# Kernel tuning notes

Hardware: AMD Instinct MI355X
Metric: run time of the kernel (lower is better)

## Reference

```python
import jax, jax.numpy as jnp
import numpy as np

HEADS, DIM_HEAD, C, B, HS, WS = 8, 64, 512, 2, 48, 48


def setup_inputs() -> dict:
    key = jax.random.key(0)
    ks = jax.random.split(key, 9)
    s = 0.02
    return {
        "hidden_states": jax.random.normal(ks[0], (B, C, HS, WS), jnp.float32),
        "Wq": jax.random.normal(ks[1], (HEADS, DIM_HEAD, C), jnp.float32) * s,
        "bq": jax.random.normal(ks[2], (HEADS, DIM_HEAD), jnp.float32) * s,
        "Wk": jax.random.normal(ks[3], (HEADS, DIM_HEAD, C), jnp.float32) * s,
        "bk": jax.random.normal(ks[4], (HEADS, DIM_HEAD), jnp.float32) * s,
        "Wv": jax.random.normal(ks[5], (HEADS, DIM_HEAD, C), jnp.float32) * s,
        "bv": jax.random.normal(ks[6], (HEADS, DIM_HEAD), jnp.float32) * s,
        "Wo": jax.random.normal(ks[7], (C, HEADS * DIM_HEAD), jnp.float32) * s,
        "bo": jax.random.normal(ks[8], (C,), jnp.float32) * s,
    }


def reference(hidden_states, Wq, bq, Wk, bk, Wv, bv, Wo, bo):
    # hidden_states: [B, C, H, W]; per-head 1x1 convs == per-head linear over C.
    b, c, h, w = hidden_states.shape
    hw = h * w
    x = hidden_states.reshape(b, c, hw)  # [B, C, HW]
    # Batched per-head projections (fuses the per-head Conv2d loop).
    q = jnp.einsum('bcs,ndc->bnsd', x, Wq) + bq[None, :, None, :]  # [B, n, HW, d]
    k = jnp.einsum('bcs,ndc->bnsd', x, Wk) + bk[None, :, None, :]
    v = jnp.einsum('bcs,ndc->bnsd', x, Wv) + bv[None, :, None, :]
    scale = 1.0 / jnp.sqrt(jnp.asarray(DIM_HEAD, hidden_states.dtype))
    scores = jnp.einsum('bnqd,bnkd->bnqk', q, k) * scale  # [B, n, HW, HW]
    probs = jax.nn.softmax(scores, axis=-1)
    attn = jnp.einsum('bnqk,bnkd->bnqd', probs, v)  # [B, n, HW, d]
    # concat heads along last dim (matches torch.cat(..., dim=-1))
    attn = attn.transpose(0, 2, 1, 3).reshape(b, hw, HEADS * DIM_HEAD)
    out = attn @ Wo.T + bo  # [B, HW, C] (to_out[0]; to_out[1] dropout = identity)
    out = out.reshape(b, h, w, c).transpose(0, 3, 1, 2)  # [B, C, H, W]
    return out
```

## Files before the change

kernel.cpp:

```cpp
#include <hip/hip_runtime.h>
#include <hip/hip_bf16.h>

#define HEADS 8
#define DHEAD 64
#define CDIM  512
#define SEQ   2304
#define ND    512
#define NCHUNK 4

typedef unsigned short u16;
typedef unsigned int   u32;
typedef __attribute__((ext_vector_type(8))) short short8;
typedef __attribute__((ext_vector_type(4))) float f32x4;

#define QSCALE 0.18033688011112043f

__device__ __forceinline__ u16 f2bf(float f) {
    union { float f; u32 u; } x; x.f = f;
    u32 r = x.u + 0x7FFFu + ((x.u >> 16) & 1u);
    return (u16)(r >> 16);
}
__device__ __forceinline__ float bf2f(u16 v) {
    union { u32 u; float f; } x; x.u = ((u32)v) << 16; return x.f;
}
__device__ __forceinline__ u32 pkbf(float a, float b) {
    union { float f; u32 u; } x, y; x.f = a; y.f = b;
    return __builtin_amdgcn_perm(y.u + 0x8000u, x.u + 0x8000u, 0x07060302u);
}
__device__ __forceinline__ u32 cvtpk(float lo, float hi) {
    u32 r;
    asm("v_cvt_pk_bf16_f32 %0, %1, %2" : "=v"(r) : "v"(lo), "v"(hi));
    return r;
}
__device__ __forceinline__ f32x4 mfma16(short8 a, short8 b, f32x4 c) {
    return __builtin_amdgcn_mfma_f32_16x16x32_bf16(a, b, c, 0, 0, 0);
}
__device__ __forceinline__ void cp16(const void* g, void* l) {
    __builtin_amdgcn_global_load_lds(
        (const __attribute__((address_space(1))) u32*)(uintptr_t)g,
        (__attribute__((address_space(3))) u32*)(u32)(uintptr_t)l,
        16, 0, 0);
}
__device__ __forceinline__ int kperm_inv(int r) {
    return (r & ~0x1C) | ((r & 0x0C) << 1) | ((r & 0x10) >> 2);
}

__global__ void prep_kernel(const float* __restrict__ H,
                            const float* __restrict__ Wq, const float* __restrict__ Wk,
                            const float* __restrict__ Wv, const float* __restrict__ Wo,
                            u16* __restrict__ Wqkv, u16* __restrict__ Wob,
                            u16* __restrict__ X) {
    __shared__ float tile[64][65];
    const int t = threadIdx.x;
    const int bx = blockIdx.x;
    if (bx < 512) {
        const int N1 = CDIM * ND;
        int i8 = (bx * 256 + t) * 8;
        const float* src;
        u16* dst;
        if (i8 < 3 * N1) {
            src = (i8 < N1) ? &Wq[i8] : (i8 < 2 * N1 ? &Wk[i8 - N1] : &Wv[i8 - 2 * N1]);
            dst = &Wqkv[i8];
        } else {
            src = &Wo[i8 - 3 * N1];
            dst = &Wob[i8 - 3 * N1];
        }
        float4 a = *(const float4*)src;
        float4 c = *(const float4*)(src + 4);
        uint4 o;
        o.x = pkbf(a.x, a.y); o.y = pkbf(a.z, a.w);
        o.z = pkbf(c.x, c.y); o.w = pkbf(c.z, c.w);
        *(uint4*)dst = o;
    } else {
        int bb = bx - 512;
        int st = bb % 36, ct = (bb / 36) % 8, b = bb / (36 * 8);
#pragma unroll
        for (int it = 0; it < 4; ++it) {
            int cl = it * 16 + (t >> 4);
            int j4 = (t & 15) * 4;
            float4 hv = *(const float4*)&H[((size_t)(b * CDIM + ct * 64 + cl)) * SEQ + st * 64 + j4];
            tile[cl][j4 + 0] = hv.x; tile[cl][j4 + 1] = hv.y;
            tile[cl][j4 + 2] = hv.z; tile[cl][j4 + 3] = hv.w;
        }
        __syncthreads();
        int sl = t >> 2, c16 = (t & 3) * 16;
        uint4 o1, o2;
        o1.x = cvtpk(tile[c16 +  0][sl], tile[c16 +  1][sl]);
        o1.y = cvtpk(tile[c16 +  2][sl], tile[c16 +  3][sl]);
        o1.z = cvtpk(tile[c16 +  4][sl], tile[c16 +  5][sl]);
        o1.w = cvtpk(tile[c16 +  6][sl], tile[c16 +  7][sl]);
        o2.x = cvtpk(tile[c16 +  8][sl], tile[c16 +  9][sl]);
        o2.y = cvtpk(tile[c16 + 10][sl], tile[c16 + 11][sl]);
        o2.z = cvtpk(tile[c16 + 12][sl], tile[c16 + 13][sl]);
        o2.w = cvtpk(tile[c16 + 14][sl], tile[c16 + 15][sl]);
        u16* xp = &X[((size_t)(b * SEQ + st * 64 + sl)) * CDIM + ct * 64 + c16];
        *(uint4*)xp = o1;
        *(uint4*)(xp + 8) = o2;
    }
}

__global__ __launch_bounds__(256, 2) void gemm_qkv_kernel(
        const u16* __restrict__ W, const u16* __restrict__ X,
        const float* __restrict__ bq, const float* __restrict__ bk, const float* __restrict__ bv,
        u16* __restrict__ Q, u16* __restrict__ K, u16* __restrict__ V) {
    __shared__ __align__(16) u16 sm[2 * (128 * 64 + 128 * 64)];
    const int n0 = blockIdx.x * 128;
    const int m0 = blockIdx.y * 128;
    const int b  = blockIdx.z;
    const int t = threadIdx.x;
    const int lane = t & 63, w = t >> 6;
    const int l16 = lane & 15, quad = lane >> 4;
    const int x7 = l16 & 7;
    const int srow = t >> 3, scol = (t & 7) * 8;
    const int scol_sw = ((t & 7) ^ (srow & 7)) * 8;
    const u16* Xb = X + (size_t)b * SEQ * CDIM;

    f32x4 acc[8][2] = {};

    {
        u16* As = sm; u16* Bs = sm + 8192;
#pragma unroll
        for (int it = 0; it < 4; ++it) {
            int r2 = it * 32 + srow;
            cp16(&W [(size_t)(m0 + r2) * 512 + scol_sw], &As[r2 * 64 + scol]);
            cp16(&Xb[(size_t)(n0 + r2) * 512 + scol_sw], &Bs[r2 * 64 + scol]);
        }
    }
    for (int kb = 0; kb < 512; kb += 64) {
        const int pb = (kb >> 6) & 1;
        const u16* As = sm + pb * 16384;
        const u16* Bs = As + 8192;
        __syncthreads();
        if (kb + 64 < 512) {
            u16* An = sm + (pb ^ 1) * 16384;
            u16* Bn = An + 8192;
#pragma unroll
            for (int it = 0; it < 4; ++it) {
                int r2 = it * 32 + srow;
                cp16(&W [(size_t)(m0 + r2) * 512 + kb + 64 + scol_sw], &An[r2 * 64 + scol]);
                cp16(&Xb[(size_t)(n0 + r2) * 512 + kb + 64 + scol_sw], &Bn[r2 * 64 + scol]);
            }
        }
#pragma unroll
        for (int kk = 0; kk < 2; ++kk) {
            const int co = ((kk * 4 + quad) ^ x7) * 8;
            short8 af[8], bfr[2];
#pragma unroll
            for (int j = 0; j < 2; ++j)
                bfr[j] = *(const short8*)&Bs[(w * 32 + j * 16 + l16) * 64 + co];
#pragma unroll
            for (int i = 0; i < 8; ++i)
                af[i] = *(const short8*)&As[(i * 16 + l16) * 64 + co];
#pragma unroll
            for (int i = 0; i < 8; ++i)
#pragma unroll
                for (int j = 0; j < 2; ++j)
                    acc[i][j] = mfma16(af[i], bfr[j], acc[i][j]);
        }
    }

    __syncthreads();
    if (m0 < 1024) {
        const bool isQ = (m0 < 512);
        const float* bias = isQ ? bq : bk;
        const float sc = isQ ? QSCALE : 1.0f;
        const int mq = isQ ? m0 : m0 - 512;
        u16* dst = isQ ? Q : K;
        u16* qb = sm;
#pragma unroll
        for (int j = 0; j < 2; ++j) {
            int sl = w * 32 + j * 16 + l16;
#pragma unroll
            for (int i = 0; i < 8; ++i) {
                int md = i * 16 + quad * 4;
                int mm = mq + md;
                uint2 val;
                val.x = pkbf((acc[i][j][0] + bias[mm + 0]) * sc, (acc[i][j][1] + bias[mm + 1]) * sc);
                val.y = pkbf((acc[i][j][2] + bias[mm + 2]) * sc, (acc[i][j][3] + bias[mm + 3]) * sc);
                *(uint2*)&qb[sl * 136 + md] = val;
            }
        }
        __syncthreads();
#pragma unroll
        for (int it = 0; it < 8; ++it) {
            int v = it * 256 + t;
            int row = v >> 4, c8 = (v & 15) * 8;
            int hh = mq + c8;
            *(uint4*)&dst[(((size_t)(b * 8 + (hh >> 6))) * SEQ + n0 + row) * 64 + (hh & 63)] =
                *(const uint4*)&qb[row * 136 + c8];
        }
    } else {
        u16* vb = sm;
        const int mv = m0 - 1024;
#pragma unroll
        for (int j = 0; j < 2; ++j) {
            int sl = w * 32 + j * 16 + l16;
#pragma unroll
            for (int i = 0; i < 8; ++i) {
                int mb = i * 16 + quad * 4;
#pragma unroll
                for (int r = 0; r < 4; ++r)
                    vb[(mb + r) * 136 + sl] = f2bf(acc[i][j][r] + bv[mv + mb + r]);
            }
        }
        __syncthreads();
#pragma unroll
        for (int it = 0; it < 8; ++it) {
            int v = it * 256 + t;
            int row = v >> 4, ch = (v & 15) * 8;
            *(uint4*)&V[((size_t)(b * 512 + mv + row)) * SEQ + n0 + ch] =
                *(const uint4*)&vb[row * 136 + ch];
        }
    }
}

__global__ __launch_bounds__(256, 3) void attn_partial(
        const u16* __restrict__ Q,
        const u16* __restrict__ K,
        const u16* __restrict__ Vt,
        u16* __restrict__ Opart,
        float* __restrict__ Lpart) {
    __shared__ __align__(16) u16 sm[2 * 8192];
    const int pair = blockIdx.x & 15, qt = blockIdx.x >> 4;
    const int c = blockIdx.y;
    const int b = pair >> 3, h = pair & 7;
    const int t = threadIdx.x, lane = t & 63, w = t >> 6;
    const int l16 = lane & 15, quad = lane >> 4;
    const int x7 = l16 & 7;
    const int srow = t >> 3;
    const int scol = (t & 7) * 8;
    const int scol_sw = ((t & 7) ^ (srow & 7)) * 8;
    const int kinv0 = kperm_inv(srow), kinv1 = kperm_inv(32 + srow);
    const int cA = (quad ^ x7) * 8;
    const int cB = (quad ^ x7 ^ 4) * 8;

    const u16* Qg = Q + ((size_t)pair * SEQ + qt * 192) * 64;
    const int rA = w * 16 + l16;
    short8 qf[3][2];
#pragma unroll
    for (int G = 0; G < 3; ++G) {
        qf[G][0] = *(const short8*)&Qg[(size_t)(G * 64 + rA) * 64 + quad * 8];
        qf[G][1] = *(const short8*)&Qg[(size_t)(G * 64 + rA) * 64 + 32 + quad * 8];
    }

    const u16* Kg = K  + ((size_t)pair * SEQ + c * 576) * 64;
    const u16* Vg = Vt + ((size_t)(b * 512 + h * 64)) * SEQ + c * 576;

    float lacc[3] = {0.f, 0.f, 0.f};
    f32x4 o[3][4] = {};

    {
        u16* Ks = sm; u16* Vs = sm + 4096;
        cp16(&Kg[(size_t)kinv0 * 64 + scol_sw], &Ks[srow * 64 + scol]);
        cp16(&Kg[(size_t)kinv1 * 64 + scol_sw], &Ks[(32 + srow) * 64 + scol]);
        cp16(&Vg[(size_t)srow * SEQ + scol_sw],        &Vs[srow * 64 + scol]);
        cp16(&Vg[(size_t)(32 + srow) * SEQ + scol_sw], &Vs[(32 + srow) * 64 + scol]);
    }
    for (int kt = 0; kt < 9; ++kt) {
        const int pb = kt & 1;
        const u16* Ks = sm + pb * 8192;
        const u16* Vs = Ks + 4096;
        __syncthreads();
        if (kt < 8) {
            u16* Kn = sm + (pb ^ 1) * 8192;
            u16* Vn = Kn + 4096;
            cp16(&Kg[(size_t)((kt + 1) * 64 + kinv0) * 64 + scol_sw], &Kn[srow * 64 + scol]);
            cp16(&Kg[(size_t)((kt + 1) * 64 + kinv1) * 64 + scol_sw], &Kn[(32 + srow) * 64 + scol]);
            cp16(&Vg[(size_t)srow * SEQ + (kt + 1) * 64 + scol_sw],        &Vn[srow * 64 + scol]);
            cp16(&Vg[(size_t)(32 + srow) * SEQ + (kt + 1) * 64 + scol_sw], &Vn[(32 + srow) * 64 + scol]);
        }
        f32x4 sacc[3][4];
        __builtin_amdgcn_s_setprio(1);
#pragma unroll
        for (int j = 0; j < 4; ++j) {
            short8 kf0 = *(const short8*)&Ks[(j * 16 + l16) * 64 + cA];
            short8 kf1 = *(const short8*)&Ks[(j * 16 + l16) * 64 + cB];
#pragma unroll
            for (int G = 0; G < 3; ++G) {
                f32x4 z = {0.f, 0.f, 0.f, 0.f};
                z = mfma16(kf0, qf[G][0], z);
                sacc[G][j] = mfma16(kf1, qf[G][1], z);
            }
        }
        __builtin_amdgcn_s_setprio(0);
        short8 pks[3][2];
#pragma unroll
        for (int G = 0; G < 3; ++G)
#pragma unroll
            for (int j = 0; j < 4; ++j) {
                float e0 = __builtin_amdgcn_exp2f(sacc[G][j][0]);
                float e1 = __builtin_amdgcn_exp2f(sacc[G][j][1]);
                float e2 = __builtin_amdgcn_exp2f(sacc[G][j][2]);
                float e3 = __builtin_amdgcn_exp2f(sacc[G][j][3]);
                lacc[G] += (e0 + e1) + (e2 + e3);
                u32* pw = (u32*)&pks[G][j >> 1];
                pw[(j & 1) * 2 + 0] = cvtpk(e0, e1);
                pw[(j & 1) * 2 + 1] = cvtpk(e2, e3);
            }
        __builtin_amdgcn_s_setprio(1);
#pragma unroll
        for (int g = 0; g < 2; ++g) {
            const int cg = g ? cB : cA;
#pragma unroll
            for (int i = 0; i < 4; ++i) {
                short8 vf = *(const short8*)&Vs[(i * 16 + l16) * 64 + cg];
#pragma unroll
                for (int G = 0; G < 3; ++G)
                    o[G][i] = mfma16(vf, pks[G][g], o[G][i]);
            }
        }
        __builtin_amdgcn_s_setprio(0);
    }
    float linv[3];
#pragma unroll
    for (int G = 0; G < 3; ++G) {
        float lr = lacc[G];
        lr += __shfl_xor(lr, 16);
        lr += __shfl_xor(lr, 32);
        if (quad == 0) Lpart[((size_t)(c * 16 + pair)) * SEQ + qt * 192 + G * 64 + rA] = lr;
        linv[G] = 1.0f / lr;
    }
    const size_t orow = ((size_t)(c * 16 + pair)) * SEQ + qt * 192;

    __syncthreads();
#pragma unroll
    for (int G = 0; G < 3; ++G)
#pragma unroll
        for (int i = 0; i < 4; ++i) {
            uint2 pkv;
            pkv.x = cvtpk(o[G][i][0] * linv[G], o[G][i][1] * linv[G]);
            pkv.y = cvtpk(o[G][i][2] * linv[G], o[G][i][3] * linv[G]);
            *(uint2*)&sm[(G * 64 + rA) * 72 + i * 16 + quad * 4] = pkv;
        }
    __syncthreads();
#pragma unroll
    for (int it = 0; it < 6; ++it) {
        int v = it * 256 + t;
        int row = v >> 3, col = (v & 7) * 8;
        *(uint4*)&Opart[(orow + row) * 64 + col] = *(const uint4*)&sm[row * 72 + col];
    }
}

__global__ __launch_bounds__(256) void attn_combine(
        const u16* __restrict__ Opart, const float* __restrict__ Lpart,
        u16* __restrict__ At) {
    const int bid = blockIdx.x;
    const int pair = bid / 72, sb = bid % 72;
    const int t = threadIdx.x;
    const int rl = t >> 3, dg = t & 7;
    const int s = sb * 32 + rl;
    const int b = pair >> 3, h = pair & 7;
    float wc[NCHUNK], L = 0.f;
#pragma unroll
    for (int c = 0; c < NCHUNK; ++c) {
        wc[c] = Lpart[(size_t)(c * 16 + pair) * SEQ + s];
        L += wc[c];
    }
    float invL = 1.0f / L;
    float acc[8] = {};
#pragma unroll
    for (int c = 0; c < NCHUNK; ++c) {
        uint4 v = *(const uint4*)&Opart[((size_t)(c * 16 + pair) * SEQ + s) * 64 + dg * 8];
        const u16* pv = (const u16*)&v;
#pragma unroll
        for (int e = 0; e < 8; ++e)
            acc[e] += wc[c] * bf2f(pv[e]);
    }
    uint4 outv;
    outv.x = pkbf(acc[0] * invL, acc[1] * invL);
    outv.y = pkbf(acc[2] * invL, acc[3] * invL);
    outv.z = pkbf(acc[4] * invL, acc[5] * invL);
    outv.w = pkbf(acc[6] * invL, acc[7] * invL);
    *(uint4*)&At[((size_t)b * SEQ + s) * ND + h * 64 + dg * 8] = outv;
}

__global__ __launch_bounds__(256) void gemm_out_kernel(
        const u16* __restrict__ Wob, const u16* __restrict__ At,
        const float* __restrict__ bo, float* __restrict__ out) {
    __shared__ __align__(16) u16 sm[2 * 8192];
    const int n0 = blockIdx.x * 64;
    const int m0 = blockIdx.y * 64;
    const int b  = blockIdx.z;
    const int t = threadIdx.x;
    const int lane = t & 63, w = t >> 6;
    const int l16 = lane & 15, quad = lane >> 4;
    const int x7 = l16 & 7;
    const int srow = t >> 3, scol = (t & 7) * 8;
    const int scol_sw = ((t & 7) ^ (srow & 7)) * 8;
    const u16* Ab = At + (size_t)b * SEQ * ND;

    f32x4 acc[4] = {};

    {
        u16* As = sm; u16* Bs = sm + 4096;
#pragma unroll
        for (int it = 0; it < 2; ++it) {
            int r2 = it * 32 + srow;
            cp16(&Wob[(size_t)(m0 + r2) * 512 + scol_sw], &As[r2 * 64 + scol]);
            cp16(&Ab [(size_t)(n0 + r2) * 512 + scol_sw], &Bs[r2 * 64 + scol]);
        }
    }
    for (int kb = 0; kb < 512; kb += 64) {
        const int pb = (kb >> 6) & 1;
        const u16* As = sm + pb * 8192;
        const u16* Bs = As + 4096;
        __syncthreads();
        if (kb + 64 < 512) {
            u16* An = sm + (pb ^ 1) * 8192;
            u16* Bn = An + 4096;
#pragma unroll
            for (int it = 0; it < 2; ++it) {
                int r2 = it * 32 + srow;
                cp16(&Wob[(size_t)(m0 + r2) * 512 + kb + 64 + scol_sw], &An[r2 * 64 + scol]);
                cp16(&Ab [(size_t)(n0 + r2) * 512 + kb + 64 + scol_sw], &Bn[r2 * 64 + scol]);
            }
        }
#pragma unroll
        for (int kk = 0; kk < 2; ++kk) {
            const int co = ((kk * 4 + quad) ^ x7) * 8;
            short8 af[4];
#pragma unroll
            for (int i = 0; i < 4; ++i)
                af[i] = *(const short8*)&As[(i * 16 + l16) * 64 + co];
            short8 bfr = *(const short8*)&Bs[(w * 16 + l16) * 64 + co];
#pragma unroll
            for (int i = 0; i < 4; ++i)
                acc[i] = mfma16(af[i], bfr, acc[i]);
        }
    }
    __syncthreads();
    float* fb = (float*)sm;
#pragma unroll
    for (int i = 0; i < 4; ++i) {
        int cl = i * 16 + quad * 4;
        int s = w * 16 + l16;
#pragma unroll
        for (int r = 0; r < 4; ++r)
            fb[(cl + r) * 68 + s] = acc[i][r] + bo[m0 + cl + r];
    }
    __syncthreads();
#pragma unroll
    for (int k2 = 0; k2 < 4; ++k2) {
        int v = k2 * 256 + t;
        int row = v >> 4, c4 = (v & 15) * 4;
        f32x4 ov = *(const f32x4*)&fb[row * 68 + c4];
        __builtin_nontemporal_store(ov, (f32x4*)&out[((size_t)(b * 512 + m0 + row)) * SEQ + n0 + c4]);
    }
}

extern "C" void kernel_launch(void* const* d_in, const int* in_sizes, int n_in,
                              void* d_out, int out_size, void* d_ws, size_t ws_size,
                              hipStream_t stream) {
    const float* H  = (const float*)d_in[0];
    const float* Wq = (const float*)d_in[1];
    const float* bq = (const float*)d_in[2];
    const float* Wk = (const float*)d_in[3];
    const float* bk = (const float*)d_in[4];
    const float* Wv = (const float*)d_in[5];
    const float* bv = (const float*)d_in[6];
    const float* Wo = (const float*)d_in[7];
    const float* bo = (const float*)d_in[8];
    float* out = (float*)d_out;

    u16* ws    = (u16*)d_ws;
    u16* Wqkv  = ws;
    u16* Wob   = Wqkv  + 1536 * 512;
    u16* Xbf   = Wob   + 512 * 512;
    u16* Qb    = Xbf   + 2 * SEQ * CDIM;
    u16* Kb    = Qb    + 2 * SEQ * ND;
    u16* Vb    = Kb    + 2 * SEQ * ND;
    u16* At    = Vb    + 2 * SEQ * ND;
    u16* Opart = At    + 2 * SEQ * ND;
    float* Lpart = (float*)(Opart + NCHUNK * 16 * SEQ * 64);

    prep_kernel<<<1088, 256, 0, stream>>>(H, Wq, Wk, Wv, Wo, Wqkv, Wob, Xbf);
    gemm_qkv_kernel<<<dim3(18, 12, 2), 256, 0, stream>>>(Wqkv, Xbf, bq, bk, bv, Qb, Kb, Vb);
    attn_partial<<<dim3(192, NCHUNK), 256, 0, stream>>>(Qb, Kb, Vb, Opart, Lpart);
    attn_combine<<<1152, 256, 0, stream>>>(Opart, Lpart, At);
    gemm_out_kernel<<<dim3(36, 8, 2), 256, 0, stream>>>(Wob, At, bo, out);
}
```

Before: 128.3 us.

## Replace split-K attention and combine kernel with single-pass attention per query tile

Drops the four-way key split and the separate combine kernel. Each block now handles 128 queries over all 2304 keys and writes normalized output directly into the concatenated-head layout. This removes the partial-output and partial-sum round trip through global memory and one kernel launch. The cost is far fewer blocks (288 instead of 768) with longer serial key loops, which leaves less concurrency per CU to hide latency and causes load imbalance on a 256-CU device.

```diff
diff --git a/kernel.cpp b/kernel.cpp
--- a/kernel.cpp
+++ b/kernel.cpp
@@ -6,7 +6,6 @@
 #define CDIM  512
 #define SEQ   2304
 #define ND    512
-#define NCHUNK 4
 
 typedef unsigned short u16;
 typedef unsigned int   u32;
@@ -214,15 +213,14 @@
     }
 }
 
-__global__ __launch_bounds__(256, 3) void attn_partial(
+__global__ __launch_bounds__(256, 3) void attn_kernel(
         const u16* __restrict__ Q,
         const u16* __restrict__ K,
         const u16* __restrict__ Vt,
-        u16* __restrict__ Opart,
-        float* __restrict__ Lpart) {
+        u16* __restrict__ At) {
     __shared__ __align__(16) u16 sm[2 * 8192];
-    const int pair = blockIdx.x & 15, qt = blockIdx.x >> 4;
-    const int c = blockIdx.y;
+    const int bx = blockIdx.x;
+    const int pair = bx / 18, qt = bx % 18;
     const int b = pair >> 3, h = pair & 7;
     const int t = threadIdx.x, lane = t & 63, w = t >> 6;
     const int l16 = lane & 15, quad = lane >> 4;
@@ -234,20 +232,20 @@
     const int cA = (quad ^ x7) * 8;
     const int cB = (quad ^ x7 ^ 4) * 8;
 
-    const u16* Qg = Q + ((size_t)pair * SEQ + qt * 192) * 64;
+    const u16* Qg = Q + ((size_t)pair * SEQ + qt * 128) * 64;
     const int rA = w * 16 + l16;
-    short8 qf[3][2];
-#pragma unroll
-    for (int G = 0; G < 3; ++G) {
+    short8 qf[2][2];
+#pragma unroll
+    for (int G = 0; G < 2; ++G) {
         qf[G][0] = *(const short8*)&Qg[(size_t)(G * 64 + rA) * 64 + quad * 8];
         qf[G][1] = *(const short8*)&Qg[(size_t)(G * 64 + rA) * 64 + 32 + quad * 8];
     }
 
-    const u16* Kg = K  + ((size_t)pair * SEQ + c * 576) * 64;
-    const u16* Vg = Vt + ((size_t)(b * 512 + h * 64)) * SEQ + c * 576;
-
-    float lacc[3] = {0.f, 0.f, 0.f};
-    f32x4 o[3][4] = {};
+    const u16* Kg = K  + (size_t)pair * SEQ * 64;
+    const u16* Vg = Vt + ((size_t)(b * 512 + h * 64)) * SEQ;
+
+    float lacc[2] = {0.f, 0.f};
+    f32x4 o[2][4] = {};
 
     {
         u16* Ks = sm; u16* Vs = sm + 4096;
@@ -256,12 +254,12 @@
         cp16(&Vg[(size_t)srow * SEQ + scol_sw],        &Vs[srow * 64 + scol]);
         cp16(&Vg[(size_t)(32 + srow) * SEQ + scol_sw], &Vs[(32 + srow) * 64 + scol]);
     }
-    for (int kt = 0; kt < 9; ++kt) {
+    for (int kt = 0; kt < 36; ++kt) {
         const int pb = kt & 1;
         const u16* Ks = sm + pb * 8192;
         const u16* Vs = Ks + 4096;
         __syncthreads();
-        if (kt < 8) {
+        if (kt < 35) {
             u16* Kn = sm + (pb ^ 1) * 8192;
             u16* Vn = Kn + 4096;
             cp16(&Kg[(size_t)((kt + 1) * 64 + kinv0) * 64 + scol_sw], &Kn[srow * 64 + scol]);
@@ -269,23 +267,23 @@
             cp16(&Vg[(size_t)srow * SEQ + (kt + 1) * 64 + scol_sw],        &Vn[srow * 64 + scol]);
             cp16(&Vg[(size_t)(32 + srow) * SEQ + (kt + 1) * 64 + scol_sw], &Vn[(32 + srow) * 64 + scol]);
         }
-        f32x4 sacc[3][4];
+        f32x4 sacc[2][4];
         __builtin_amdgcn_s_setprio(1);
 #pragma unroll
         for (int j = 0; j < 4; ++j) {
             short8 kf0 = *(const short8*)&Ks[(j * 16 + l16) * 64 + cA];
             short8 kf1 = *(const short8*)&Ks[(j * 16 + l16) * 64 + cB];
 #pragma unroll
-            for (int G = 0; G < 3; ++G) {
+            for (int G = 0; G < 2; ++G) {
                 f32x4 z = {0.f, 0.f, 0.f, 0.f};
                 z = mfma16(kf0, qf[G][0], z);
                 sacc[G][j] = mfma16(kf1, qf[G][1], z);
             }
         }
         __builtin_amdgcn_s_setprio(0);
-        short8 pks[3][2];
-#pragma unroll
-        for (int G = 0; G < 3; ++G)
+        short8 pks[2][2];
+#pragma unroll
+        for (int G = 0; G < 2; ++G)
 #pragma unroll
             for (int j = 0; j < 4; ++j) {
                 float e0 = __builtin_amdgcn_exp2f(sacc[G][j][0]);
@@ -305,26 +303,24 @@
             for (int i = 0; i < 4; ++i) {
                 short8 vf = *(const short8*)&Vs[(i * 16 + l16) * 64 + cg];
 #pragma unroll
-                for (int G = 0; G < 3; ++G)
+                for (int G = 0; G < 2; ++G)
                     o[G][i] = mfma16(vf, pks[G][g], o[G][i]);
             }
         }
         __builtin_amdgcn_s_setprio(0);
     }
-    float linv[3];
-#pragma unroll
-    for (int G = 0; G < 3; ++G) {
+    float linv[2];
+#pragma unroll
+    for (int G = 0; G < 2; ++G) {
         float lr = lacc[G];
         lr += __shfl_xor(lr, 16);
         lr += __shfl_xor(lr, 32);
-        if (quad == 0) Lpart[((size_t)(c * 16 + pair)) * SEQ + qt * 192 + G * 64 + rA] = lr;
         linv[G] = 1.0f / lr;
     }
-    const size_t orow = ((size_t)(c * 16 + pair)) * SEQ + qt * 192;
 
     __syncthreads();
 #pragma unroll
-    for (int G = 0; G < 3; ++G)
+    for (int G = 0; G < 2; ++G)
 #pragma unroll
         for (int i = 0; i < 4; ++i) {
             uint2 pkv;
@@ -334,44 +330,12 @@
         }
     __syncthreads();
 #pragma unroll
-    for (int it = 0; it < 6; ++it) {
+    for (int it = 0; it < 4; ++it) {
         int v = it * 256 + t;
         int row = v >> 3, col = (v & 7) * 8;
-        *(uint4*)&Opart[(orow + row) * 64 + col] = *(const uint4*)&sm[row * 72 + col];
-    }
-}
-
-__global__ __launch_bounds__(256) void attn_combine(
-        const u16* __restrict__ Opart, const float* __restrict__ Lpart,
-        u16* __restrict__ At) {
-    const int bid = blockIdx.x;
-    const int pair = bid / 72, sb = bid % 72;
-    const int t = threadIdx.x;
-    const int rl = t >> 3, dg = t & 7;
-    const int s = sb * 32 + rl;
-    const int b = pair >> 3, h = pair & 7;
-    float wc[NCHUNK], L = 0.f;
-#pragma unroll
-    for (int c = 0; c < NCHUNK; ++c) {
-        wc[c] = Lpart[(size_t)(c * 16 + pair) * SEQ + s];
-        L += wc[c];
-    }
-    float invL = 1.0f / L;
-    float acc[8] = {};
-#pragma unroll
-    for (int c = 0; c < NCHUNK; ++c) {
-        uint4 v = *(const uint4*)&Opart[((size_t)(c * 16 + pair) * SEQ + s) * 64 + dg * 8];
-        const u16* pv = (const u16*)&v;
-#pragma unroll
-        for (int e = 0; e < 8; ++e)
-            acc[e] += wc[c] * bf2f(pv[e]);
-    }
-    uint4 outv;
-    outv.x = pkbf(acc[0] * invL, acc[1] * invL);
-    outv.y = pkbf(acc[2] * invL, acc[3] * invL);
-    outv.z = pkbf(acc[4] * invL, acc[5] * invL);
-    outv.w = pkbf(acc[6] * invL, acc[7] * invL);
-    *(uint4*)&At[((size_t)b * SEQ + s) * ND + h * 64 + dg * 8] = outv;
+        *(uint4*)&At[((size_t)(b * SEQ) + qt * 128 + row) * ND + h * 64 + col] =
+            *(const uint4*)&sm[row * 72 + col];
+    }
 }
 
 __global__ __launch_bounds__(256) void gemm_out_kernel(
@@ -470,12 +434,9 @@
     u16* Kb    = Qb    + 2 * SEQ * ND;
     u16* Vb    = Kb    + 2 * SEQ * ND;
     u16* At    = Vb    + 2 * SEQ * ND;
-    u16* Opart = At    + 2 * SEQ * ND;
-    float* Lpart = (float*)(Opart + NCHUNK * 16 * SEQ * 64);
 
     prep_kernel<<<1088, 256, 0, stream>>>(H, Wq, Wk, Wv, Wo, Wqkv, Wob, Xbf);
     gemm_qkv_kernel<<<dim3(18, 12, 2), 256, 0, stream>>>(Wqkv, Xbf, bq, bk, bv, Qb, Kb, Vb);
-    attn_partial<<<dim3(192, NCHUNK), 256, 0, stream>>>(Qb, Kb, Vb, Opart, Lpart);
-    attn_combine<<<1152, 256, 0, stream>>>(Opart, Lpart, At);
+    attn_kernel<<<288, 256, 0, stream>>>(Qb, Kb, Vb, At);
     gemm_out_kernel<<<dim3(36, 8, 2), 256, 0, stream>>>(Wob, At, bo, out);
 }
```

Measured after the change: 137.8 us. +7.4%, slower.
